# Optimization experiments

Hardware: AMD Instinct MI355X
Metric: run time of the kernel (lower is better)

Reference implementation:

```python
import jax, jax.numpy as jnp
import numpy as np

DN = ('NDHWC', 'DHWIO', 'NDHWC')
EPS = 1e-5  # torch BatchNorm default

def _conv(x, w, s):
    # Minkowski conv, kernel 3 centered: output coord j gathers input coords s*j + {-1,0,1}
    return jax.lax.conv_general_dilated(x, w, (s, s, s), ((1, 1),) * 3, dimension_numbers=DN)

def _convt(x, w):
    # stride-2 transpose conv, kernel 3 centered: output p gets input c where 2c in {p-1,p,p+1}
    return jax.lax.conv_general_dilated(x, w, (1, 1, 1), ((1, 2),) * 3,
                                        lhs_dilation=(2, 2, 2), dimension_numbers=DN)

def _down(m):
    # stride-2 coordinate map: a coarse voxel is active iff any of its 2x2x2 fine voxels is
    B, G = m.shape[0], m.shape[1]
    return m.reshape(B, G // 2, 2, G // 2, 2, G // 2, 2).any(axis=(2, 4, 6))

def _mbn(h, m, g, b):
    # MinkowskiBatchNorm: BatchNorm1d over the active (sparse) feature rows only
    mf = m[..., None].astype(h.dtype)
    h = h * mf
    cnt = jnp.maximum(jnp.sum(mf), 1.0)
    mean = jnp.sum(h, axis=(0, 1, 2, 3)) / cnt
    var = jnp.sum(((h - mean) * mf) ** 2, axis=(0, 1, 2, 3)) / cnt
    return ((h - mean) * jax.lax.rsqrt(var + EPS) * g + b) * mf


def setup_inputs() -> dict:
    key = jax.random.key(0)
    ks = jax.random.split(key, 8)
    B, G, Cin, Cout = 2, 64, 4, 16
    def w(k, shape, fan):
        return jax.random.normal(k, shape, jnp.float32) * np.float32(1.0 / np.sqrt(fan))
    return {
        'x': jax.random.normal(ks[0], (B, G, G, G, Cin), jnp.float32),
        'mask': jax.random.bernoulli(ks[1], 0.1, (B, G, G, G)),
        'w1': w(ks[2], (3, 3, 3, Cin, 8), 27 * Cin), 'g1': jnp.ones(8), 'b1': jnp.zeros(8),
        'w2': w(ks[3], (3, 3, 3, 8, 16), 27 * 8), 'g2': jnp.ones(16), 'b2': jnp.zeros(16),
        'w3': w(ks[4], (3, 3, 3, 16, 32), 27 * 16), 'g3': jnp.ones(32), 'b3': jnp.zeros(32),
        'w3t': w(ks[5], (3, 3, 3, 32, 16), 27 * 32), 'g3t': jnp.ones(16), 'b3t': jnp.zeros(16),
        'w2t': w(ks[6], (3, 3, 3, 32, 16), 27 * 32), 'g2t': jnp.ones(16), 'b2t': jnp.zeros(16),
        'w1x1': w(ks[7], (24, Cout), 24),
    }


def reference(x, mask, w1, g1, b1, w2, g2, b2, w3, g3, b3,
              w3t, g3t, b3t, w2t, g2t, b2t, w1x1):
    m1 = mask
    m2 = _down(m1)
    m4 = _down(m2)
    mf1 = m1[..., None].astype(x.dtype)

    xs = x * mf1                                      # sparse tensor: zero at inactive coords
    s1 = _mbn(_conv(xs, w1, 1), m1, g1, b1)           # block1, stride 1
    o = jax.nn.relu(s1)
    s2 = _mbn(_conv(o, w2, 2), m2, g2, b2)            # block2, stride 2
    o = jax.nn.relu(s2)
    s4 = _mbn(_conv(o, w3, 2), m4, g3, b3)            # block3, stride 4
    o = jax.nn.relu(s4)

    o = jax.nn.relu(_mbn(_convt(o, w3t), m2, g3t, b3t))   # block3_tr -> stride-2 coords
    o = jnp.concatenate([o, s2], axis=-1)                 # ME.cat(out, out_s2) -> 32 ch
    o = jax.nn.relu(_mbn(_convt(o, w2t), m1, g2t, b2t))   # block2_tr -> stride-1 coords
    o = jnp.concatenate([o, s1], axis=-1)                 # ME.cat(out, out_s1) -> 24 ch
    return jnp.einsum('bdhwc,co->bdhwo', o, w1x1) * mf1   # conv1_tr: 1x1x1 conv
```

## Files before the change

### kernel.cpp

```cpp
#include <hip/hip_runtime.h>

#define NVOX1 524288
#define NVOX2 65536
#define NVOX4 8192

#define ST_SUM1 16
#define ST_SQ1  24
#define ST_SUM2 32
#define ST_SQ2  48
#define ST_SUM3 64
#define ST_SQ3  96
#define ST_SUM3T 128
#define ST_SQ3T  144
#define ST_SUM2T 160
#define ST_SQ2T  176
#define FLAG_OFF 200
#define IC_N1 204
#define IC_N2 205
#define IC_N4 206
#define ST_ZERO 256

#define OFF_M1C 512
#define OFF_M2  (OFF_M1C + NVOX1)
#define OFF_M4  (OFF_M2 + NVOX2)
#define OFF_H1  (OFF_M4 + NVOX4)
#define OFF_S2  (OFF_H1 + NVOX1 * 8)
#define OFF_H3  (OFF_S2 + NVOX2 * 16)
#define OFF_T3  (OFF_H3 + NVOX4 * 32)
#define OFF_L1  (OFF_T3 + NVOX2 * 16)
#define OFF_L2  (OFF_L1 + NVOX1)
#define OFF_L4  (OFF_L2 + NVOX2)
#define OFF_BC1 (OFF_L4 + NVOX4)
#define OFF_BC2 (OFF_BC1 + 2048)
#define OFF_BC4 (OFF_BC2 + 256)

#define EPSBN 1e-5f

__device__ __forceinline__ void ttaps(int p, int gin, int* c, int* k, int* ok) {
  c[0] = p >> 1; k[0] = (p & 1) ? 0 : 1; ok[0] = 1;
  int cb = (p + 1) >> 1;
  int o = (p & 1) && (cb < gin);
  c[1] = o ? cb : 0; k[1] = 2; ok[1] = o;
}

__device__ __forceinline__ void stat_flush8(float* sum, float* sq, float* s_sum, float* s_sq, int t) {
#pragma unroll
  for (int off = 1; off < 64; off <<= 1)
#pragma unroll
    for (int c = 0; c < 8; c++) {
      sum[c] += __shfl_xor(sum[c], off, 64);
      sq[c]  += __shfl_xor(sq[c], off, 64);
    }
  if ((t & 63) == 0) {
#pragma unroll
    for (int c = 0; c < 8; c++) { atomicAdd(&s_sum[c], sum[c]); atomicAdd(&s_sq[c], sq[c]); }
  }
}

__global__ __launch_bounds__(256) void k_detect(const unsigned int* __restrict__ m,
                                                int* __restrict__ flags) {
  int tid = blockIdx.x * 256 + threadIdx.x;
  int hasf = 0, hasb = 0;
  for (int i = tid; i < NVOX1; i += 256 * 256) {
    unsigned int v = m[i];
    if (v == 0x3F800000u) hasf = 1;
    else if (v > 1u) hasb = 1;
  }
  hasf = __syncthreads_or(hasf);
  hasb = __syncthreads_or(hasb);
  if (threadIdx.x == 0) {
    if (hasf) atomicOr(&flags[0], 1);
    if (hasb) atomicOr(&flags[1], 1);
  }
}

__global__ __launch_bounds__(256) void k_canon(const void* __restrict__ mraw,
                                               int* __restrict__ m1c,
                                               const int* __restrict__ flags,
                                               int* __restrict__ blkcnt1) {
  int idx = blockIdx.x * 256 + threadIdx.x;
  int isf = flags[0], isb = flags[1];
  int v;
  if (isf)      v = (((const float*)mraw)[idx] != 0.f);
  else if (isb) v = (((const unsigned char*)mraw)[idx] != 0);
  else          v = (((const int*)mraw)[idx] != 0);
  m1c[idx] = v;
  int c = __syncthreads_count(v);
  if (threadIdx.x == 0) blkcnt1[blockIdx.x] = c;
}

__global__ __launch_bounds__(256) void k_down1(const int* __restrict__ m1,
                                               int* __restrict__ m2,
                                               int* __restrict__ blkcnt2) {
  int idx = blockIdx.x * 256 + threadIdx.x;
  int x = idx & 31, y = (idx >> 5) & 31, z = (idx >> 10) & 31, b = idx >> 15;
  int any = 0;
#pragma unroll
  for (int dz = 0; dz < 2; dz++)
#pragma unroll
    for (int dy = 0; dy < 2; dy++)
#pragma unroll
      for (int dx = 0; dx < 2; dx++)
        any |= m1[((b * 64 + 2 * z + dz) * 64 + 2 * y + dy) * 64 + 2 * x + dx];
  any = any ? 1 : 0;
  m2[idx] = any;
  int c = __syncthreads_count(any);
  if (threadIdx.x == 0) blkcnt2[blockIdx.x] = c;
}

__global__ __launch_bounds__(256) void k_down2(const int* __restrict__ m2,
                                               int* __restrict__ m4,
                                               int* __restrict__ blkcnt4) {
  int idx = blockIdx.x * 256 + threadIdx.x;
  int x = idx & 15, y = (idx >> 4) & 15, z = (idx >> 8) & 15, b = idx >> 12;
  int any = 0;
#pragma unroll
  for (int dz = 0; dz < 2; dz++)
#pragma unroll
    for (int dy = 0; dy < 2; dy++)
#pragma unroll
      for (int dx = 0; dx < 2; dx++)
        any |= m2[((b * 32 + 2 * z + dz) * 32 + 2 * y + dy) * 32 + 2 * x + dx];
  any = any ? 1 : 0;
  m4[idx] = any;
  int c = __syncthreads_count(any);
  if (threadIdx.x == 0) blkcnt4[blockIdx.x] = c;
}

__global__ __launch_bounds__(1024) void k_scan(int* __restrict__ bc1,
                                               int* __restrict__ bc2,
                                               int* __restrict__ bc4,
                                               int* __restrict__ cnts) {
  __shared__ int sA[2048], sB[2048];
  int* a; int n; int outIdx;
  if (blockIdx.x == 0)      { a = bc1; n = 2048; outIdx = IC_N1; }
  else if (blockIdx.x == 1) { a = bc2; n = 256;  outIdx = IC_N2; }
  else                      { a = bc4; n = 32;   outIdx = IC_N4; }
  int t = threadIdx.x;
  int i0 = t, i1 = t + 1024;
  int v0 = (i0 < n) ? a[i0] : 0;
  int v1 = (i1 < n) ? a[i1] : 0;
  sA[i0] = v0; sA[i1] = v1;
  __syncthreads();
  int* src = sA; int* dst = sB;
  for (int st = 1; st < 2048; st <<= 1) {
    int x0 = src[i0]; if (i0 >= st) x0 += src[i0 - st];
    int x1 = src[i1]; if (i1 >= st) x1 += src[i1 - st];
    dst[i0] = x0; dst[i1] = x1;
    __syncthreads();
    int* tmp = src; src = dst; dst = tmp;
  }
  if (i0 < n) a[i0] = src[i0] - v0;
  if (i1 < n) a[i1] = src[i1] - v1;
  if (t == 0) cnts[outIdx] = src[2047];
}

__global__ __launch_bounds__(256) void k_scatter(const int* __restrict__ m1,
                                                 const int* __restrict__ m2,
                                                 const int* __restrict__ m4,
                                                 const int* __restrict__ bc1,
                                                 const int* __restrict__ bc2,
                                                 const int* __restrict__ bc4,
                                                 int* __restrict__ list1,
                                                 int* __restrict__ list2,
                                                 int* __restrict__ list4) {
  __shared__ int s_w[4];
  int bid = blockIdx.x, t = threadIdx.x;
  const int* mask; const int* base; int* list; int lb;
  if (bid < 2048)      { mask = m1; base = bc1; list = list1; lb = bid; }
  else if (bid < 2304) { mask = m2; base = bc2; list = list2; lb = bid - 2048; }
  else                 { mask = m4; base = bc4; list = list4; lb = bid - 2304; }
  int idx = lb * 256 + t;
  int act = mask[idx];
  unsigned long long b = __ballot(act != 0);
  int lane = t & 63, wid = t >> 6;
  if (lane == 0) s_w[wid] = __popcll(b);
  __syncthreads();
  int wbase = 0;
  for (int i = 0; i < wid; i++) wbase += s_w[i];
  if (act) {
    int pre = __popcll(b & ((1ull << lane) - 1ull));
    list[base[lb] + wbase + pre] = idx;
  }
}

__global__ __launch_bounds__(256) void k_conv1(const float* __restrict__ x,
                                               const int* __restrict__ m1,
                                               const int* __restrict__ list1,
                                               const int* __restrict__ cnts,
                                               const float* __restrict__ w,
                                               float* __restrict__ h1,
                                               float* __restrict__ stats) {
  __shared__ float s_w[27 * 32];
  __shared__ float s_sum[8], s_sq[8];
  int t = threadIdx.x;
  { const float4* w4 = (const float4*)w; float4* sw4 = (float4*)s_w;
    for (int i = t; i < 216; i += 256) sw4[i] = w4[i]; }
  if (t < 8) { s_sum[t] = 0.f; s_sq[t] = 0.f; }
  __syncthreads();
  int n = cnts[IC_N1];
  float sum[8], sq[8];
#pragma unroll
  for (int c = 0; c < 8; c++) { sum[c] = 0.f; sq[c] = 0.f; }
  for (int i = blockIdx.x * 256 + t; i < n; i += gridDim.x * 256) {
    int v = list1[i];
    int vx = v & 63, vy = (v >> 6) & 63, vz = (v >> 12) & 63, vb = v >> 18;
    float acc[8];
#pragma unroll
    for (int c = 0; c < 8; c++) acc[c] = 0.f;
#pragma unroll
    for (int kd = 0; kd < 3; kd++) { int d = vz + kd - 1; if ((unsigned)d >= 64u) continue;
#pragma unroll
      for (int kh = 0; kh < 3; kh++) { int h = vy + kh - 1; if ((unsigned)h >= 64u) continue;
#pragma unroll
        for (int kw = 0; kw < 3; kw++) { int ww = vx + kw - 1; if ((unsigned)ww >= 64u) continue;
          int ni = ((vb * 64 + d) * 64 + h) * 64 + ww;
          if (!m1[ni]) continue;
          float4 ip = *(const float4*)(x + (size_t)ni * 4);
          const float* wp = s_w + ((kd * 3 + kh) * 3 + kw) * 32;
#pragma unroll
          for (int co = 0; co < 8; co++) {
            float a = fmaf(ip.x, wp[co], acc[co]);
            a = fmaf(ip.y, wp[8 + co], a);
            a = fmaf(ip.z, wp[16 + co], a);
            acc[co] = fmaf(ip.w, wp[24 + co], a);
          }
        } } }
    float4* hp = (float4*)(h1 + (size_t)v * 8);
    float4 q0 = {acc[0], acc[1], acc[2], acc[3]};
    float4 q1 = {acc[4], acc[5], acc[6], acc[7]};
    hp[0] = q0; hp[1] = q1;
#pragma unroll
    for (int c = 0; c < 8; c++) { sum[c] += acc[c]; sq[c] += acc[c] * acc[c]; }
  }
  stat_flush8(sum, sq, s_sum, s_sq, t);
  __syncthreads();
  if (t < 8) {
    if (s_sum[t] != 0.f) atomicAdd(&stats[ST_SUM1 + t], s_sum[t]);
    if (s_sq[t]  != 0.f) atomicAdd(&stats[ST_SQ1 + t], s_sq[t]);
  }
}

__global__ __launch_bounds__(256) void k_conv2(const float* __restrict__ h1,
                                               const int* __restrict__ m1,
                                               const int* __restrict__ list2,
                                               const int* __restrict__ cnts,
                                               const float* __restrict__ w,
                                               const float* __restrict__ g1,
                                               const float* __restrict__ b1,
                                               float* __restrict__ s2,
                                               float* __restrict__ stats) {
  __shared__ float s_w[27 * 8 * 8];
  __shared__ float s_sc[8], s_bi[8];
  __shared__ float s_sum[8], s_sq[8];
  int t = threadIdx.x, g = blockIdx.y;
  for (int i = t; i < 432; i += 256) {
    int r = i >> 1, half = i & 1;
    *(float4*)(s_w + r * 8 + half * 4) = *(const float4*)(w + r * 16 + g * 8 + half * 4);
  }
  if (t < 8) {
    float cnt = fmaxf((float)cnts[IC_N1], 1.f);
    float mean = stats[ST_SUM1 + t] / cnt;
    float var = fmaxf(stats[ST_SQ1 + t] / cnt - mean * mean, 0.f);
    float sc = g1[t] * rsqrtf(var + EPSBN);
    s_sc[t] = sc; s_bi[t] = b1[t] - mean * sc;
    s_sum[t] = 0.f; s_sq[t] = 0.f;
  }
  __syncthreads();
  int n = cnts[IC_N2];
  float sum[8], sq[8];
#pragma unroll
  for (int c = 0; c < 8; c++) { sum[c] = 0.f; sq[c] = 0.f; }
  for (int i = blockIdx.x * 256 + t; i < n; i += gridDim.x * 256) {
    int v = list2[i];
    int vx = v & 31, vy = (v >> 5) & 31, vz = (v >> 10) & 31, vb = v >> 15;
    float acc[8];
#pragma unroll
    for (int c = 0; c < 8; c++) acc[c] = 0.f;
#pragma unroll
    for (int kd = 0; kd < 3; kd++) { int d = 2 * vz + kd - 1; if (d < 0) continue;
#pragma unroll
      for (int kh = 0; kh < 3; kh++) { int h = 2 * vy + kh - 1; if (h < 0) continue;
#pragma unroll
        for (int kw = 0; kw < 3; kw++) { int ww = 2 * vx + kw - 1; if (ww < 0) continue;
          int ni = ((vb * 64 + d) * 64 + h) * 64 + ww;
          if (!m1[ni]) continue;
          float4 i0 = *(const float4*)(h1 + (size_t)ni * 8);
          float4 i1 = *(const float4*)(h1 + (size_t)ni * 8 + 4);
          float r[8] = {i0.x, i0.y, i0.z, i0.w, i1.x, i1.y, i1.z, i1.w};
          const float* wp = s_w + ((kd * 3 + kh) * 3 + kw) * 64;
#pragma unroll
          for (int ci = 0; ci < 8; ci++) {
            float vv = fmaxf(fmaf(r[ci], s_sc[ci], s_bi[ci]), 0.f);
#pragma unroll
            for (int co = 0; co < 8; co++) acc[co] = fmaf(vv, wp[ci * 8 + co], acc[co]);
          }
        } } }
    float4* sp = (float4*)(s2 + (size_t)v * 16 + g * 8);
    float4 q0 = {acc[0], acc[1], acc[2], acc[3]};
    float4 q1 = {acc[4], acc[5], acc[6], acc[7]};
    sp[0] = q0; sp[1] = q1;
#pragma unroll
    for (int c = 0; c < 8; c++) { sum[c] += acc[c]; sq[c] += acc[c] * acc[c]; }
  }
  stat_flush8(sum, sq, s_sum, s_sq, t);
  __syncthreads();
  if (t < 8) {
    if (s_sum[t] != 0.f) atomicAdd(&stats[ST_SUM2 + g * 8 + t], s_sum[t]);
    if (s_sq[t]  != 0.f) atomicAdd(&stats[ST_SQ2 + g * 8 + t], s_sq[t]);
  }
}

__global__ __launch_bounds__(256) void k_conv3(const float* __restrict__ s2raw,
                                               const int* __restrict__ m2,
                                               const int* __restrict__ list4,
                                               const int* __restrict__ cnts,
                                               const float* __restrict__ w,
                                               const float* __restrict__ g2,
                                               const float* __restrict__ b2,
                                               float* __restrict__ h3,
                                               float* __restrict__ stats) {
  __shared__ float s_w[27 * 16 * 8];
  __shared__ float s_sc[16], s_bi[16];
  __shared__ float s_sum[8], s_sq[8];
  int t = threadIdx.x, g = blockIdx.y;
  for (int i = t; i < 864; i += 256) {
    int r = i >> 1, half = i & 1;
    *(float4*)(s_w + r * 8 + half * 4) = *(const float4*)(w + r * 32 + g * 8 + half * 4);
  }
  if (t < 16) {
    float cnt = fmaxf((float)cnts[IC_N2], 1.f);
    float mean = stats[ST_SUM2 + t] / cnt;
    float var = fmaxf(stats[ST_SQ2 + t] / cnt - mean * mean, 0.f);
    float sc = g2[t] * rsqrtf(var + EPSBN);
    s_sc[t] = sc; s_bi[t] = b2[t] - mean * sc;
  }
  if (t < 8) { s_sum[t] = 0.f; s_sq[t] = 0.f; }
  __syncthreads();
  int n = cnts[IC_N4];
  float sum[8], sq[8];
#pragma unroll
  for (int c = 0; c < 8; c++) { sum[c] = 0.f; sq[c] = 0.f; }
  for (int i = blockIdx.x * 256 + t; i < n; i += gridDim.x * 256) {
    int v = list4[i];
    int vx = v & 15, vy = (v >> 4) & 15, vz = (v >> 8) & 15, vb = v >> 12;
    float acc[8];
#pragma unroll
    for (int c = 0; c < 8; c++) acc[c] = 0.f;
#pragma unroll
    for (int kd = 0; kd < 3; kd++) { int d = 2 * vz + kd - 1; if (d < 0) continue;
#pragma unroll
      for (int kh = 0; kh < 3; kh++) { int h = 2 * vy + kh - 1; if (h < 0) continue;
#pragma unroll
        for (int kw = 0; kw < 3; kw++) { int ww = 2 * vx + kw - 1; if (ww < 0) continue;
          int ni = ((vb * 32 + d) * 32 + h) * 32 + ww;
          if (!m2[ni]) continue;
          const float4* ip = (const float4*)(s2raw + (size_t)ni * 16);
          const float* wp = s_w + ((kd * 3 + kh) * 3 + kw) * 128;
#pragma unroll
          for (int cq = 0; cq < 4; cq++) {
            float4 q = ip[cq];
            float rr[4] = {q.x, q.y, q.z, q.w};
#pragma unroll
            for (int j = 0; j < 4; j++) {
              int ci = cq * 4 + j;
              float vv = fmaxf(fmaf(rr[j], s_sc[ci], s_bi[ci]), 0.f);
#pragma unroll
              for (int co = 0; co < 8; co++) acc[co] = fmaf(vv, wp[ci * 8 + co], acc[co]);
            }
          }
        } } }
    float4* hp = (float4*)(h3 + (size_t)v * 32 + g * 8);
    float4 q0 = {acc[0], acc[1], acc[2], acc[3]};
    float4 q1 = {acc[4], acc[5], acc[6], acc[7]};
    hp[0] = q0; hp[1] = q1;
#pragma unroll
    for (int c = 0; c < 8; c++) { sum[c] += acc[c]; sq[c] += acc[c] * acc[c]; }
  }
  stat_flush8(sum, sq, s_sum, s_sq, t);
  __syncthreads();
  if (t < 8) {
    if (s_sum[t] != 0.f) atomicAdd(&stats[ST_SUM3 + g * 8 + t], s_sum[t]);
    if (s_sq[t]  != 0.f) atomicAdd(&stats[ST_SQ3 + g * 8 + t], s_sq[t]);
  }
}

__global__ __launch_bounds__(256) void k_convt3(const float* __restrict__ h3raw,
                                                const int* __restrict__ m4,
                                                const int* __restrict__ list2,
                                                const int* __restrict__ cnts,
                                                const float* __restrict__ w,
                                                const float* __restrict__ g3,
                                                const float* __restrict__ b3,
                                                float* __restrict__ t3,
                                                float* __restrict__ stats) {
  __shared__ float s_w[27 * 32 * 8];
  __shared__ float s_sc[32], s_bi[32];
  __shared__ float s_sum[8], s_sq[8];
  int t = threadIdx.x, g = blockIdx.y;
  for (int i = t; i < 1728; i += 256) {
    int r = i >> 1, half = i & 1;
    *(float4*)(s_w + r * 8 + half * 4) = *(const float4*)(w + r * 16 + g * 8 + half * 4);
  }
  if (t < 32) {
    float cnt = fmaxf((float)cnts[IC_N4], 1.f);
    float mean = stats[ST_SUM3 + t] / cnt;
    float var = fmaxf(stats[ST_SQ3 + t] / cnt - mean * mean, 0.f);
    float sc = g3[t] * rsqrtf(var + EPSBN);
    s_sc[t] = sc; s_bi[t] = b3[t] - mean * sc;
  }
  if (t < 8) { s_sum[t] = 0.f; s_sq[t] = 0.f; }
  __syncthreads();
  int n = cnts[IC_N2];
  float sum[8], sq[8];
#pragma unroll
  for (int c = 0; c < 8; c++) { sum[c] = 0.f; sq[c] = 0.f; }
  for (int i = blockIdx.x * 256 + t; i < n; i += gridDim.x * 256) {
    int v = list2[i];
    int px = v & 31, py = (v >> 5) & 31, pz = (v >> 10) & 31, vb = v >> 15;
    int czv[2], kzv[2], okz[2], cyv[2], kyv[2], oky[2], cxv[2], kxv[2], okx[2];
    ttaps(pz, 16, czv, kzv, okz);
    ttaps(py, 16, cyv, kyv, oky);
    ttaps(px, 16, cxv, kxv, okx);
    float acc[8];
#pragma unroll
    for (int c = 0; c < 8; c++) acc[c] = 0.f;
#pragma unroll
    for (int dz = 0; dz < 2; dz++)
#pragma unroll
      for (int dy = 0; dy < 2; dy++)
#pragma unroll
        for (int dx = 0; dx < 2; dx++) {
          if (!(okz[dz] & oky[dy] & okx[dx])) continue;
          int ni = ((vb * 16 + czv[dz]) * 16 + cyv[dy]) * 16 + cxv[dx];
          if (!m4[ni]) continue;
          const float4* ip = (const float4*)(h3raw + (size_t)ni * 32);
          const float* wp = s_w + ((kzv[dz] * 3 + kyv[dy]) * 3 + kxv[dx]) * 256;
#pragma unroll
          for (int cq = 0; cq < 8; cq++) {
            float4 q = ip[cq];
            float rr[4] = {q.x, q.y, q.z, q.w};
#pragma unroll
            for (int j = 0; j < 4; j++) {
              int ci = cq * 4 + j;
              float vv = fmaxf(fmaf(rr[j], s_sc[ci], s_bi[ci]), 0.f);
#pragma unroll
              for (int co = 0; co < 8; co++) acc[co] = fmaf(vv, wp[ci * 8 + co], acc[co]);
            }
          }
        }
    float4* op = (float4*)(t3 + (size_t)v * 16 + g * 8);
    float4 q0 = {acc[0], acc[1], acc[2], acc[3]};
    float4 q1 = {acc[4], acc[5], acc[6], acc[7]};
    op[0] = q0; op[1] = q1;
#pragma unroll
    for (int c = 0; c < 8; c++) { sum[c] += acc[c]; sq[c] += acc[c] * acc[c]; }
  }
  stat_flush8(sum, sq, s_sum, s_sq, t);
  __syncthreads();
  if (t < 8) {
    if (s_sum[t] != 0.f) atomicAdd(&stats[ST_SUM3T + g * 8 + t], s_sum[t]);
    if (s_sq[t]  != 0.f) atomicAdd(&stats[ST_SQ3T + g * 8 + t], s_sq[t]);
  }
}

__global__ __launch_bounds__(256) void k_convt2(const float* __restrict__ t3raw,
                                                const float* __restrict__ s2raw,
                                                const int* __restrict__ m2,
                                                const int* __restrict__ list1,
                                                const int* __restrict__ cnts,
                                                const float* __restrict__ w,
                                                const float* __restrict__ g3t,
                                                const float* __restrict__ b3t,
                                                const float* __restrict__ g2,
                                                const float* __restrict__ b2,
                                                float* __restrict__ outraw,
                                                float* __restrict__ stats) {
  __shared__ float s_w[27 * 32 * 8];
  __shared__ float s_sct[16], s_bit[16], s_sc2[16], s_bi2[16];
  __shared__ float s_sum[8], s_sq[8];
  int t = threadIdx.x, g = blockIdx.y;
  for (int i = t; i < 1728; i += 256) {
    int r = i >> 1, half = i & 1;
    *(float4*)(s_w + r * 8 + half * 4) = *(const float4*)(w + r * 16 + g * 8 + half * 4);
  }
  if (t < 16) {
    float cnt = fmaxf((float)cnts[IC_N2], 1.f);
    float mean = stats[ST_SUM3T + t] / cnt;
    float var = fmaxf(stats[ST_SQ3T + t] / cnt - mean * mean, 0.f);
    float sc = g3t[t] * rsqrtf(var + EPSBN);
    s_sct[t] = sc; s_bit[t] = b3t[t] - mean * sc;
    float mean2 = stats[ST_SUM2 + t] / cnt;
    float var2 = fmaxf(stats[ST_SQ2 + t] / cnt - mean2 * mean2, 0.f);
    float sc2 = g2[t] * rsqrtf(var2 + EPSBN);
    s_sc2[t] = sc2; s_bi2[t] = b2[t] - mean2 * sc2;
  }
  if (t < 8) { s_sum[t] = 0.f; s_sq[t] = 0.f; }
  __syncthreads();
  int n = cnts[IC_N1];
  float sum[8], sq[8];
#pragma unroll
  for (int c = 0; c < 8; c++) { sum[c] = 0.f; sq[c] = 0.f; }
  for (int i = blockIdx.x * 256 + t; i < n; i += gridDim.x * 256) {
    int v = list1[i];
    int px = v & 63, py = (v >> 6) & 63, pz = (v >> 12) & 63, vb = v >> 18;
    int czv[2], kzv[2], okz[2], cyv[2], kyv[2], oky[2], cxv[2], kxv[2], okx[2];
    ttaps(pz, 32, czv, kzv, okz);
    ttaps(py, 32, cyv, kyv, oky);
    ttaps(px, 32, cxv, kxv, okx);
    float acc[8];
#pragma unroll
    for (int c = 0; c < 8; c++) acc[c] = 0.f;
#pragma unroll
    for (int dz = 0; dz < 2; dz++)
#pragma unroll
      for (int dy = 0; dy < 2; dy++)
#pragma unroll
        for (int dx = 0; dx < 2; dx++) {
          if (!(okz[dz] & oky[dy] & okx[dx])) continue;
          int ni = ((vb * 32 + czv[dz]) * 32 + cyv[dy]) * 32 + cxv[dx];
          if (!m2[ni]) continue;
          const float4* tp = (const float4*)(t3raw + (size_t)ni * 16);
          const float4* sp = (const float4*)(s2raw + (size_t)ni * 16);
          const float* wp = s_w + ((kzv[dz] * 3 + kyv[dy]) * 3 + kxv[dx]) * 256;
#pragma unroll
          for (int cq = 0; cq < 4; cq++) {
            float4 q = tp[cq];
            float rr[4] = {q.x, q.y, q.z, q.w};
#pragma unroll
            for (int j = 0; j < 4; j++) {
              int ci = cq * 4 + j;
              float vv = fmaxf(fmaf(rr[j], s_sct[ci], s_bit[ci]), 0.f);
#pragma unroll
              for (int co = 0; co < 8; co++) acc[co] = fmaf(vv, wp[ci * 8 + co], acc[co]);
            }
          }
#pragma unroll
          for (int cq = 0; cq < 4; cq++) {
            float4 q = sp[cq];
            float rr[4] = {q.x, q.y, q.z, q.w};
#pragma unroll
            for (int j = 0; j < 4; j++) {
              int ci = cq * 4 + j;
              float vv = fmaf(rr[j], s_sc2[ci], s_bi2[ci]);
#pragma unroll
              for (int co = 0; co < 8; co++) acc[co] = fmaf(vv, wp[(16 + ci) * 8 + co], acc[co]);
            }
          }
        }
    float4* op = (float4*)(outraw + (size_t)v * 16 + g * 8);
    float4 q0 = {acc[0], acc[1], acc[2], acc[3]};
    float4 q1 = {acc[4], acc[5], acc[6], acc[7]};
    op[0] = q0; op[1] = q1;
#pragma unroll
    for (int c = 0; c < 8; c++) { sum[c] += acc[c]; sq[c] += acc[c] * acc[c]; }
  }
  stat_flush8(sum, sq, s_sum, s_sq, t);
  __syncthreads();
  if (t < 8) {
    if (s_sum[t] != 0.f) atomicAdd(&stats[ST_SUM2T + g * 8 + t], s_sum[t]);
    if (s_sq[t]  != 0.f) atomicAdd(&stats[ST_SQ2T + g * 8 + t], s_sq[t]);
  }
}

__global__ __launch_bounds__(256) void k_final(float* __restrict__ out,
                                               const float* __restrict__ h1raw,
                                               const int* __restrict__ list1,
                                               const int* __restrict__ cnts,
                                               const float* __restrict__ g2t,
                                               const float* __restrict__ b2t,
                                               const float* __restrict__ g1,
                                               const float* __restrict__ b1,
                                               const float* __restrict__ w1x1,
                                               const float* __restrict__ stats) {
  __shared__ float s_sc[16], s_bi[16], s_sc1[8], s_bi1[8], s_w[384];
  int t = threadIdx.x;
  for (int i = t; i < 384; i += 256) s_w[i] = w1x1[i];
  if (t < 16) {
    float cnt = fmaxf((float)cnts[IC_N1], 1.f);
    float mean = stats[ST_SUM2T + t] / cnt;
    float var = fmaxf(stats[ST_SQ2T + t] / cnt - mean * mean, 0.f);
    float sc = g2t[t] * rsqrtf(var + EPSBN);
    s_sc[t] = sc; s_bi[t] = b2t[t] - mean * sc;
  }
  if (t < 8) {
    float cnt = fmaxf((float)cnts[IC_N1], 1.f);
    float mean = stats[ST_SUM1 + t] / cnt;
    float var = fmaxf(stats[ST_SQ1 + t] / cnt - mean * mean, 0.f);
    float sc = g1[t] * rsqrtf(var + EPSBN);
    s_sc1[t] = sc; s_bi1[t] = b1[t] - mean * sc;
  }
  __syncthreads();
  int n = cnts[IC_N1];
  for (int i = blockIdx.x * 256 + t; i < n; i += gridDim.x * 256) {
    int v = list1[i];
    float* op = out + (size_t)v * 16;
    float t2[16];
    {
      const float4* op4 = (const float4*)op;
#pragma unroll
      for (int cq = 0; cq < 4; cq++) {
        float4 q = op4[cq];
        t2[cq * 4 + 0] = fmaxf(fmaf(q.x, s_sc[cq * 4 + 0], s_bi[cq * 4 + 0]), 0.f);
        t2[cq * 4 + 1] = fmaxf(fmaf(q.y, s_sc[cq * 4 + 1], s_bi[cq * 4 + 1]), 0.f);
        t2[cq * 4 + 2] = fmaxf(fmaf(q.z, s_sc[cq * 4 + 2], s_bi[cq * 4 + 2]), 0.f);
        t2[cq * 4 + 3] = fmaxf(fmaf(q.w, s_sc[cq * 4 + 3], s_bi[cq * 4 + 3]), 0.f);
      }
    }
    float s1v[8];
    {
      const float4* sp4 = (const float4*)(h1raw + (size_t)v * 8);
#pragma unroll
      for (int cq = 0; cq < 2; cq++) {
        float4 q = sp4[cq];
        s1v[cq * 4 + 0] = fmaf(q.x, s_sc1[cq * 4 + 0], s_bi1[cq * 4 + 0]);
        s1v[cq * 4 + 1] = fmaf(q.y, s_sc1[cq * 4 + 1], s_bi1[cq * 4 + 1]);
        s1v[cq * 4 + 2] = fmaf(q.z, s_sc1[cq * 4 + 2], s_bi1[cq * 4 + 2]);
        s1v[cq * 4 + 3] = fmaf(q.w, s_sc1[cq * 4 + 3], s_bi1[cq * 4 + 3]);
      }
    }
    float o[16];
#pragma unroll
    for (int oc = 0; oc < 16; oc++) o[oc] = 0.f;
#pragma unroll
    for (int c = 0; c < 16; c++) {
      float vv = t2[c];
#pragma unroll
      for (int oc = 0; oc < 16; oc++) o[oc] = fmaf(vv, s_w[c * 16 + oc], o[oc]);
    }
#pragma unroll
    for (int c = 0; c < 8; c++) {
      float vv = s1v[c];
#pragma unroll
      for (int oc = 0; oc < 16; oc++) o[oc] = fmaf(vv, s_w[(16 + c) * 16 + oc], o[oc]);
    }
    float4* op4 = (float4*)op;
#pragma unroll
    for (int cq = 0; cq < 4; cq++) {
      float4 q = {o[cq * 4 + 0], o[cq * 4 + 1], o[cq * 4 + 2], o[cq * 4 + 3]};
      op4[cq] = q;
    }
  }
}

extern "C" void kernel_launch(void* const* d_in, const int* in_sizes, int n_in,
                              void* d_out, int out_size, void* d_ws, size_t ws_size,
                              hipStream_t stream) {
  const float* x    = (const float*)d_in[0];
  const void*  mraw = d_in[1];
  const float* w1   = (const float*)d_in[2];
  const float* g1   = (const float*)d_in[3];
  const float* b1   = (const float*)d_in[4];
  const float* w2   = (const float*)d_in[5];
  const float* g2   = (const float*)d_in[6];
  const float* b2   = (const float*)d_in[7];
  const float* w3   = (const float*)d_in[8];
  const float* g3   = (const float*)d_in[9];
  const float* b3   = (const float*)d_in[10];
  const float* w3t  = (const float*)d_in[11];
  const float* g3t  = (const float*)d_in[12];
  const float* b3t  = (const float*)d_in[13];
  const float* w2t  = (const float*)d_in[14];
  const float* g2t  = (const float*)d_in[15];
  const float* b2t  = (const float*)d_in[16];
  const float* w1x1 = (const float*)d_in[17];

  float* ws = (float*)d_ws;
  float* stats = ws;
  int* cnts = (int*)ws;
  int* flags = (int*)(ws + FLAG_OFF);
  int* m1c = (int*)(ws + OFF_M1C);
  int* m2  = (int*)(ws + OFF_M2);
  int* m4  = (int*)(ws + OFF_M4);
  float* h1 = ws + OFF_H1;
  float* s2 = ws + OFF_S2;
  float* h3 = ws + OFF_H3;
  float* t3 = ws + OFF_T3;
  int* list1 = (int*)(ws + OFF_L1);
  int* list2 = (int*)(ws + OFF_L2);
  int* list4 = (int*)(ws + OFF_L4);
  int* bc1 = (int*)(ws + OFF_BC1);
  int* bc2 = (int*)(ws + OFF_BC2);
  int* bc4 = (int*)(ws + OFF_BC4);
  float* out = (float*)d_out;

  hipMemsetAsync(ws, 0, ST_ZERO * sizeof(float), stream);
  hipMemsetAsync(d_out, 0, (size_t)out_size * sizeof(float), stream);
  k_detect<<<256, 256, 0, stream>>>((const unsigned int*)mraw, flags);
  k_canon<<<NVOX1 / 256, 256, 0, stream>>>(mraw, m1c, flags, bc1);
  k_down1<<<NVOX2 / 256, 256, 0, stream>>>(m1c, m2, bc2);
  k_down2<<<NVOX4 / 256, 256, 0, stream>>>(m2, m4, bc4);
  k_scan<<<3, 1024, 0, stream>>>(bc1, bc2, bc4, cnts);
  k_scatter<<<2048 + 256 + 32, 256, 0, stream>>>(m1c, m2, m4, bc1, bc2, bc4, list1, list2, list4);
  k_conv1<<<256, 256, 0, stream>>>(x, m1c, list1, cnts, w1, h1, stats);
  k_conv2<<<dim3(256, 2), 256, 0, stream>>>(h1, m1c, list2, cnts, w2, g1, b1, s2, stats);
  k_conv3<<<dim3(32, 4), 256, 0, stream>>>(s2, m2, list4, cnts, w3, g2, b2, h3, stats);
  k_convt3<<<dim3(256, 2), 256, 0, stream>>>(h3, m4, list2, cnts, w3t, g3, b3, t3, stats);
  k_convt2<<<dim3(256, 2), 256, 0, stream>>>(t3, s2, m2, list1, cnts, w2t, g3t, b3t, g2, b2, out, stats);
  k_final<<<256, 256, 0, stream>>>(out, h1, list1, cnts, g2t, b2t, g1, b1, w1x1, stats);
}
```

Baseline: 197.3 us.

## Fold output zeroing into dense final pass; add occupancy hints and drop tap unrolling

Removes the separate memset of the full output buffer. The final 1x1 kernel now runs densely over all voxels, writing zeros at inactive ones and computing the result at active ones. This relies on convt2 writing only active rows, so inactive rows must not be read before being zeroed. It also adds launch_bounds min-blocks hints to the conv kernels and removes full unrolling of the 27-tap loops to lower register pressure, at the cost of loop overhead.

```diff
diff --git a/kernel.cpp b/kernel.cpp
--- a/kernel.cpp
+++ b/kernel.cpp
@@ -184,13 +184,13 @@
   }
 }
 
-__global__ __launch_bounds__(256) void k_conv1(const float* __restrict__ x,
-                                               const int* __restrict__ m1,
-                                               const int* __restrict__ list1,
-                                               const int* __restrict__ cnts,
-                                               const float* __restrict__ w,
-                                               float* __restrict__ h1,
-                                               float* __restrict__ stats) {
+__global__ __launch_bounds__(256, 4) void k_conv1(const float* __restrict__ x,
+                                                  const int* __restrict__ m1,
+                                                  const int* __restrict__ list1,
+                                                  const int* __restrict__ cnts,
+                                                  const float* __restrict__ w,
+                                                  float* __restrict__ h1,
+                                                  float* __restrict__ stats) {
   __shared__ float s_w[27 * 32];
   __shared__ float s_sum[8], s_sq[8];
   int t = threadIdx.x;
@@ -208,11 +208,8 @@
     float acc[8];
 #pragma unroll
     for (int c = 0; c < 8; c++) acc[c] = 0.f;
-#pragma unroll
     for (int kd = 0; kd < 3; kd++) { int d = vz + kd - 1; if ((unsigned)d >= 64u) continue;
-#pragma unroll
       for (int kh = 0; kh < 3; kh++) { int h = vy + kh - 1; if ((unsigned)h >= 64u) continue;
-#pragma unroll
         for (int kw = 0; kw < 3; kw++) { int ww = vx + kw - 1; if ((unsigned)ww >= 64u) continue;
           int ni = ((vb * 64 + d) * 64 + h) * 64 + ww;
           if (!m1[ni]) continue;
@@ -241,15 +238,15 @@
   }
 }
 
-__global__ __launch_bounds__(256) void k_conv2(const float* __restrict__ h1,
-                                               const int* __restrict__ m1,
-                                               const int* __restrict__ list2,
-                                               const int* __restrict__ cnts,
-                                               const float* __restrict__ w,
-                                               const float* __restrict__ g1,
-                                               const float* __restrict__ b1,
-                                               float* __restrict__ s2,
-                                               float* __restrict__ stats) {
+__global__ __launch_bounds__(256, 4) void k_conv2(const float* __restrict__ h1,
+                                                  const int* __restrict__ m1,
+                                                  const int* __restrict__ list2,
+                                                  const int* __restrict__ cnts,
+                                                  const float* __restrict__ w,
+                                                  const float* __restrict__ g1,
+                                                  const float* __restrict__ b1,
+                                                  float* __restrict__ s2,
+                                                  float* __restrict__ stats) {
   __shared__ float s_w[27 * 8 * 8];
   __shared__ float s_sc[8], s_bi[8];
   __shared__ float s_sum[8], s_sq[8];
@@ -277,11 +274,8 @@
     float acc[8];
 #pragma unroll
     for (int c = 0; c < 8; c++) acc[c] = 0.f;
-#pragma unroll
     for (int kd = 0; kd < 3; kd++) { int d = 2 * vz + kd - 1; if (d < 0) continue;
-#pragma unroll
       for (int kh = 0; kh < 3; kh++) { int h = 2 * vy + kh - 1; if (h < 0) continue;
-#pragma unroll
         for (int kw = 0; kw < 3; kw++) { int ww = 2 * vx + kw - 1; if (ww < 0) continue;
           int ni = ((vb * 64 + d) * 64 + h) * 64 + ww;
           if (!m1[ni]) continue;
@@ -311,15 +305,15 @@
   }
 }
 
-__global__ __launch_bounds__(256) void k_conv3(const float* __restrict__ s2raw,
-                                               const int* __restrict__ m2,
-                                               const int* __restrict__ list4,
-                                               const int* __restrict__ cnts,
-                                               const float* __restrict__ w,
-                                               const float* __restrict__ g2,
-                                               const float* __restrict__ b2,
-                                               float* __restrict__ h3,
-                                               float* __restrict__ stats) {
+__global__ __launch_bounds__(256, 4) void k_conv3(const float* __restrict__ s2raw,
+                                                  const int* __restrict__ m2,
+                                                  const int* __restrict__ list4,
+                                                  const int* __restrict__ cnts,
+                                                  const float* __restrict__ w,
+                                                  const float* __restrict__ g2,
+                                                  const float* __restrict__ b2,
+                                                  float* __restrict__ h3,
+                                                  float* __restrict__ stats) {
   __shared__ float s_w[27 * 16 * 8];
   __shared__ float s_sc[16], s_bi[16];
   __shared__ float s_sum[8], s_sq[8];
@@ -347,11 +341,8 @@
     float acc[8];
 #pragma unroll
     for (int c = 0; c < 8; c++) acc[c] = 0.f;
-#pragma unroll
     for (int kd = 0; kd < 3; kd++) { int d = 2 * vz + kd - 1; if (d < 0) continue;
-#pragma unroll
       for (int kh = 0; kh < 3; kh++) { int h = 2 * vy + kh - 1; if (h < 0) continue;
-#pragma unroll
         for (int kw = 0; kw < 3; kw++) { int ww = 2 * vx + kw - 1; if (ww < 0) continue;
           int ni = ((vb * 32 + d) * 32 + h) * 32 + ww;
           if (!m2[ni]) continue;
@@ -385,15 +376,15 @@
   }
 }
 
-__global__ __launch_bounds__(256) void k_convt3(const float* __restrict__ h3raw,
-                                                const int* __restrict__ m4,
-                                                const int* __restrict__ list2,
-                                                const int* __restrict__ cnts,
-                                                const float* __restrict__ w,
-                                                const float* __restrict__ g3,
-                                                const float* __restrict__ b3,
-                                                float* __restrict__ t3,
-                                                float* __restrict__ stats) {
+__global__ __launch_bounds__(256, 4) void k_convt3(const float* __restrict__ h3raw,
+                                                   const int* __restrict__ m4,
+                                                   const int* __restrict__ list2,
+                                                   const int* __restrict__ cnts,
+                                                   const float* __restrict__ w,
+                                                   const float* __restrict__ g3,
+                                                   const float* __restrict__ b3,
+                                                   float* __restrict__ t3,
+                                                   float* __restrict__ stats) {
   __shared__ float s_w[27 * 32 * 8];
   __shared__ float s_sc[32], s_bi[32];
   __shared__ float s_sum[8], s_sq[8];
@@ -464,18 +455,18 @@
   }
 }
 
-__global__ __launch_bounds__(256) void k_convt2(const float* __restrict__ t3raw,
-                                                const float* __restrict__ s2raw,
-                                                const int* __restrict__ m2,
-                                                const int* __restrict__ list1,
-                                                const int* __restrict__ cnts,
-                                                const float* __restrict__ w,
-                                                const float* __restrict__ g3t,
-                                                const float* __restrict__ b3t,
-                                                const float* __restrict__ g2,
-                                                const float* __restrict__ b2,
-                                                float* __restrict__ outraw,
-                                                float* __restrict__ stats) {
+__global__ __launch_bounds__(256, 4) void k_convt2(const float* __restrict__ t3raw,
+                                                   const float* __restrict__ s2raw,
+                                                   const int* __restrict__ m2,
+                                                   const int* __restrict__ list1,
+                                                   const int* __restrict__ cnts,
+                                                   const float* __restrict__ w,
+                                                   const float* __restrict__ g3t,
+                                                   const float* __restrict__ b3t,
+                                                   const float* __restrict__ g2,
+                                                   const float* __restrict__ b2,
+                                                   float* __restrict__ outraw,
+                                                   float* __restrict__ stats) {
   __shared__ float s_w[27 * 32 * 8];
   __shared__ float s_sct[16], s_bit[16], s_sc2[16], s_bi2[16];
   __shared__ float s_sum[8], s_sq[8];
@@ -565,7 +556,7 @@
 
 __global__ __launch_bounds__(256) void k_final(float* __restrict__ out,
                                                const float* __restrict__ h1raw,
-                                               const int* __restrict__ list1,
+                                               const int* __restrict__ m1,
                                                const int* __restrict__ cnts,
                                                const float* __restrict__ g2t,
                                                const float* __restrict__ b2t,
@@ -591,55 +582,56 @@
     s_sc1[t] = sc; s_bi1[t] = b1[t] - mean * sc;
   }
   __syncthreads();
-  int n = cnts[IC_N1];
-  for (int i = blockIdx.x * 256 + t; i < n; i += gridDim.x * 256) {
-    int v = list1[i];
-    float* op = out + (size_t)v * 16;
-    float t2[16];
-    {
-      const float4* op4 = (const float4*)op;
-#pragma unroll
-      for (int cq = 0; cq < 4; cq++) {
-        float4 q = op4[cq];
-        t2[cq * 4 + 0] = fmaxf(fmaf(q.x, s_sc[cq * 4 + 0], s_bi[cq * 4 + 0]), 0.f);
-        t2[cq * 4 + 1] = fmaxf(fmaf(q.y, s_sc[cq * 4 + 1], s_bi[cq * 4 + 1]), 0.f);
-        t2[cq * 4 + 2] = fmaxf(fmaf(q.z, s_sc[cq * 4 + 2], s_bi[cq * 4 + 2]), 0.f);
-        t2[cq * 4 + 3] = fmaxf(fmaf(q.w, s_sc[cq * 4 + 3], s_bi[cq * 4 + 3]), 0.f);
-      }
+  int v = blockIdx.x * 256 + t;
+  float* op = out + (size_t)v * 16;
+  float4* op4 = (float4*)op;
+  if (!m1[v]) {
+    float4 z = {0.f, 0.f, 0.f, 0.f};
+    op4[0] = z; op4[1] = z; op4[2] = z; op4[3] = z;
+    return;
+  }
+  float t2[16];
+  {
+#pragma unroll
+    for (int cq = 0; cq < 4; cq++) {
+      float4 q = op4[cq];
+      t2[cq * 4 + 0] = fmaxf(fmaf(q.x, s_sc[cq * 4 + 0], s_bi[cq * 4 + 0]), 0.f);
+      t2[cq * 4 + 1] = fmaxf(fmaf(q.y, s_sc[cq * 4 + 1], s_bi[cq * 4 + 1]), 0.f);
+      t2[cq * 4 + 2] = fmaxf(fmaf(q.z, s_sc[cq * 4 + 2], s_bi[cq * 4 + 2]), 0.f);
+      t2[cq * 4 + 3] = fmaxf(fmaf(q.w, s_sc[cq * 4 + 3], s_bi[cq * 4 + 3]), 0.f);
     }
-    float s1v[8];
-    {
-      const float4* sp4 = (const float4*)(h1raw + (size_t)v * 8);
-#pragma unroll
-      for (int cq = 0; cq < 2; cq++) {
-        float4 q = sp4[cq];
-        s1v[cq * 4 + 0] = fmaf(q.x, s_sc1[cq * 4 + 0], s_bi1[cq * 4 + 0]);
-        s1v[cq * 4 + 1] = fmaf(q.y, s_sc1[cq * 4 + 1], s_bi1[cq * 4 + 1]);
-        s1v[cq * 4 + 2] = fmaf(q.z, s_sc1[cq * 4 + 2], s_bi1[cq * 4 + 2]);
-        s1v[cq * 4 + 3] = fmaf(q.w, s_sc1[cq * 4 + 3], s_bi1[cq * 4 + 3]);
-      }
+  }
+  float s1v[8];
+  {
+    const float4* sp4 = (const float4*)(h1raw + (size_t)v * 8);
+#pragma unroll
+    for (int cq = 0; cq < 2; cq++) {
+      float4 q = sp4[cq];
+      s1v[cq * 4 + 0] = fmaf(q.x, s_sc1[cq * 4 + 0], s_bi1[cq * 4 + 0]);
+      s1v[cq * 4 + 1] = fmaf(q.y, s_sc1[cq * 4 + 1], s_bi1[cq * 4 + 1]);
+      s1v[cq * 4 + 2] = fmaf(q.z, s_sc1[cq * 4 + 2], s_bi1[cq * 4 + 2]);
+      s1v[cq * 4 + 3] = fmaf(q.w, s_sc1[cq * 4 + 3], s_bi1[cq * 4 + 3]);
     }
-    float o[16];
-#pragma unroll
-    for (int oc = 0; oc < 16; oc++) o[oc] = 0.f;
-#pragma unroll
-    for (int c = 0; c < 16; c++) {
-      float vv = t2[c];
-#pragma unroll
-      for (int oc = 0; oc < 16; oc++) o[oc] = fmaf(vv, s_w[c * 16 + oc], o[oc]);
-    }
-#pragma unroll
-    for (int c = 0; c < 8; c++) {
-      float vv = s1v[c];
-#pragma unroll
-      for (int oc = 0; oc < 16; oc++) o[oc] = fmaf(vv, s_w[(16 + c) * 16 + oc], o[oc]);
-    }
-    float4* op4 = (float4*)op;
-#pragma unroll
-    for (int cq = 0; cq < 4; cq++) {
-      float4 q = {o[cq * 4 + 0], o[cq * 4 + 1], o[cq * 4 + 2], o[cq * 4 + 3]};
-      op4[cq] = q;
-    }
+  }
+  float o[16];
+#pragma unroll
+  for (int oc = 0; oc < 16; oc++) o[oc] = 0.f;
+#pragma unroll
+  for (int c = 0; c < 16; c++) {
+    float vv = t2[c];
+#pragma unroll
+    for (int oc = 0; oc < 16; oc++) o[oc] = fmaf(vv, s_w[c * 16 + oc], o[oc]);
+  }
+#pragma unroll
+  for (int c = 0; c < 8; c++) {
+    float vv = s1v[c];
+#pragma unroll
+    for (int oc = 0; oc < 16; oc++) o[oc] = fmaf(vv, s_w[(16 + c) * 16 + oc], o[oc]);
+  }
+#pragma unroll
+  for (int cq = 0; cq < 4; cq++) {
+    float4 q = {o[cq * 4 + 0], o[cq * 4 + 1], o[cq * 4 + 2], o[cq * 4 + 3]};
+    op4[cq] = q;
   }
 }
 
@@ -685,7 +677,6 @@
   float* out = (float*)d_out;
 
   hipMemsetAsync(ws, 0, ST_ZERO * sizeof(float), stream);
-  hipMemsetAsync(d_out, 0, (size_t)out_size * sizeof(float), stream);
   k_detect<<<256, 256, 0, stream>>>((const unsigned int*)mraw, flags);
   k_canon<<<NVOX1 / 256, 256, 0, stream>>>(mraw, m1c, flags, bc1);
   k_down1<<<NVOX2 / 256, 256, 0, stream>>>(m1c, m2, bc2);
@@ -697,5 +688,5 @@
   k_conv3<<<dim3(32, 4), 256, 0, stream>>>(s2, m2, list4, cnts, w3, g2, b2, h3, stats);
   k_convt3<<<dim3(256, 2), 256, 0, stream>>>(h3, m4, list2, cnts, w3t, g3, b3, t3, stats);
   k_convt2<<<dim3(256, 2), 256, 0, stream>>>(t3, s2, m2, list1, cnts, w2t, g3t, b3t, g2, b2, out, stats);
-  k_final<<<256, 256, 0, stream>>>(out, h1, list1, cnts, g2t, b2t, g1, b1, w1x1, stats);
-}
+  k_final<<<NVOX1 / 256, 256, 0, stream>>>(out, h1, m1c, cnts, g2t, b2t, g1, b1, w1x1, stats);
+}
```

Result: slower. 255.0 us (+29.3%).
